# Performance work log

Hardware: AMD Instinct MI355X
Metric: run time of the kernel (lower is better)

Reference implementation:

```python
import jax, jax.numpy as jnp
import numpy as np

EPS_LN = 1e-5   # torch.nn.LayerNorm default eps
EPS_Q = 1e-5    # BitNetQuantizer eps
QMAX = 127.0    # 2**(8-1) - 1 for 8-bit activations


def _layernorm(v):
    # LayerNorm without affine params, biased variance (torch default)
    mu = jnp.mean(v, axis=-1, keepdims=True)
    var = jnp.var(v, axis=-1, keepdims=True)
    return (v - mu) / jnp.sqrt(var + EPS_LN)


def setup_inputs() -> dict:
    key = jax.random.key(0)
    k1, k2, k3 = jax.random.split(key, 3)
    B, S, DIN, DOUT = 4, 4096, 2048, 2048
    x = jax.random.normal(k1, (B, S, DIN), dtype=jnp.float32)
    # ternary weights in {-1, 0, +1}
    weight_ternary = jax.random.randint(k2, (DOUT, DIN), -1, 2, dtype=jnp.int32)
    # positive per-row scale (from_float uses a scalar expanded; per-row is the stored form)
    weight_scale = jax.random.uniform(k3, (DOUT,), dtype=jnp.float32, minval=0.01, maxval=0.05)
    return {"x": x, "weight_ternary": weight_ternary, "weight_scale": weight_scale}


def reference(x, weight_ternary, weight_scale):
    # input LayerNorm (no affine)
    xn = _layernorm(x)
    # 8-bit activation quantization: per-token absmax scale
    x_scale = jnp.clip(jnp.max(jnp.abs(xn), axis=-1, keepdims=True), EPS_Q, None) / QMAX
    x_quant = jnp.clip(jnp.round(xn / x_scale), -QMAX, QMAX)
    x_float = x_quant * x_scale  # [B, S, DIN]
    # dequantize ternary weights: [DOUT, DIN]
    w = weight_ternary.astype(jnp.float32) * weight_scale[:, None]
    # F.linear: x @ w.T
    out = jnp.einsum('bsi,oi->bso', x_float, w)
    # output LayerNorm (no affine)
    return _layernorm(out)
```

## Files before the change

### kernel.cpp

```cpp
#include <hip/hip_runtime.h>
#include <hip/hip_bf16.h>
#include <stdint.h>

using int32x4 = __attribute__((ext_vector_type(4))) int;

#define DIN 2048
#define DOUT 2048
#define NTOK 16384
#define KDIM 2048
#define NDIM 2048

#define BM 256
#define BN 256
#define BKB 64
#define NKT (KDIM / BKB)
#define TILEB (BM * BKB)

typedef const __attribute__((address_space(1))) void* gp_t;
typedef __attribute__((address_space(3))) void* lp_t;

__device__ __forceinline__ void gload16(const void* g, void* l) {
    __builtin_amdgcn_global_load_lds((gp_t)g, (lp_t)l, 16, 0, 0);
}

__global__ __launch_bounds__(256) void k_wconv(const int* __restrict__ wt,
                                               signed char* __restrict__ w8) {
    int i = blockIdx.x * 256 + threadIdx.x;
    int4 v = ((const int4*)wt)[i];
    char4 c;
    c.x = (signed char)v.x; c.y = (signed char)v.y;
    c.z = (signed char)v.z; c.w = (signed char)v.w;
    ((char4*)w8)[i] = c;
}

__global__ __launch_bounds__(256) void k_lnq(const float* __restrict__ x,
                                             signed char* __restrict__ xq,
                                             float* __restrict__ xscale) {
    __shared__ float sm[12];
    const int row = blockIdx.x;
    const int tid = threadIdx.x;
    const float* p = x + (size_t)row * DIN;
    const float4 v0 = ((const float4*)p)[tid * 2];
    const float4 v1 = ((const float4*)p)[tid * 2 + 1];
    float vv[8] = {v0.x, v0.y, v0.z, v0.w, v1.x, v1.y, v1.z, v1.w};
    float s = 0.f, ss = 0.f;
#pragma unroll
    for (int i = 0; i < 8; i++) { s += vv[i]; ss += vv[i] * vv[i]; }
#pragma unroll
    for (int o = 32; o; o >>= 1) { s += __shfl_down(s, o); ss += __shfl_down(ss, o); }
    const int wv = tid >> 6;
    if ((tid & 63) == 0) { sm[wv] = s; sm[4 + wv] = ss; }
    __syncthreads();
    s = sm[0] + sm[1] + sm[2] + sm[3];
    ss = sm[4] + sm[5] + sm[6] + sm[7];
    const float mu = s * (1.f / DIN);
    const float var = ss * (1.f / DIN) - mu * mu;
    const float rstd = 1.f / sqrtf(var + 1e-5f);
    float am = 0.f;
#pragma unroll
    for (int i = 0; i < 8; i++) am = fmaxf(am, fabsf(vv[i] - mu));
#pragma unroll
    for (int o = 32; o; o >>= 1) am = fmaxf(am, __shfl_down(am, o));
    __syncthreads();
    if ((tid & 63) == 0) sm[8 + wv] = am;
    __syncthreads();
    am = fmaxf(fmaxf(sm[8], sm[9]), fmaxf(sm[10], sm[11]));
    const float scale = fmaxf(am * rstd, 1e-5f) * (1.f / 127.f);
    union { signed char c[8]; int2 v; } u;
#pragma unroll
    for (int i = 0; i < 8; i++) {
        float xn = (vv[i] - mu) * rstd;
        float t = rintf(xn / scale);
        t = fminf(127.f, fmaxf(-127.f, t));
        u.c[i] = (signed char)t;
    }
    ((int2*)(xq + (size_t)row * DIN))[tid] = u.v;
    if (tid == 0) xscale[row] = scale;
}

#define MFMA4(I, AF) \
    acc[I][0] = __builtin_amdgcn_mfma_i32_16x16x64_i8(AF, b0, acc[I][0], 0, 0, 0); \
    acc[I][1] = __builtin_amdgcn_mfma_i32_16x16x64_i8(AF, b1, acc[I][1], 0, 0, 0); \
    acc[I][2] = __builtin_amdgcn_mfma_i32_16x16x64_i8(AF, b2, acc[I][2], 0, 0, 0); \
    acc[I][3] = __builtin_amdgcn_mfma_i32_16x16x64_i8(AF, b3, acc[I][3], 0, 0, 0);

#define SCHED __builtin_amdgcn_sched_barrier(0);
#define BAR   __builtin_amdgcn_s_barrier();

__global__ __launch_bounds__(512, 2) void k_gemm(const signed char* __restrict__ A,
                                                 const signed char* __restrict__ B,
                                                 const float* __restrict__ xs,
                                                 const float* __restrict__ wsc,
                                                 float* __restrict__ C) {
    __shared__ __align__(16) signed char lA[3][TILEB];
    __shared__ __align__(16) signed char lB[3][TILEB];
    __shared__ float s_xs[BM];
    __shared__ float s_ws[BN];

    const int tid = threadIdx.x;
    const int orig = blockIdx.x;
    const int bid = (orig & 7) * 64 + (orig >> 3);
    const int bm = bid >> 3;
    const int bn = bid & 7;

    const int lane = tid & 63;
    const int wave = tid >> 6;
    const int wm = wave >> 2;
    const int wn = wave & 3;
    const int lo = lane & 15;
    const int q  = lane >> 4;

    const int srow = tid >> 2;
    const int gch  = (tid & 3) ^ ((srow >> 1) & 3);
    const signed char* gA = A + (size_t)(bm * BM + srow) * KDIM + gch * 16;
    const signed char* gB = B + (size_t)(bn * BN + srow) * KDIM + gch * 16;
    const int dst = tid * 16;

    const int slot = (q ^ ((lo >> 1) & 3)) * 16;
    const int abase = (wm * 128 + lo) * BKB + slot;
    const int bbase = (wn * 64 + lo) * BKB + slot;

    if (tid < 256) s_xs[tid] = xs[bm * BM + tid];
    else           s_ws[tid - 256] = wsc[bn * BN + tid - 256];

#define STAGE_A(T, BUF) \
    gload16(gA + (T) * BKB,                        &lA[BUF][0] + dst); \
    gload16(gA + (T) * BKB + (size_t)128 * KDIM,   &lA[BUF][0] + dst + 8192);
#define STAGE_B(T, BUF) \
    gload16(gB + (T) * BKB,                        &lB[BUF][0] + dst); \
    gload16(gB + (T) * BKB + (size_t)128 * KDIM,   &lB[BUF][0] + dst + 8192);

    STAGE_A(0, 0) STAGE_B(0, 0)
    STAGE_A(1, 1) STAGE_B(1, 1)
    asm volatile("s_waitcnt vmcnt(0)" ::: "memory");
    SCHED BAR SCHED

    int32x4 acc[8][4];
#pragma unroll
    for (int i = 0; i < 8; i++)
#pragma unroll
        for (int j = 0; j < 4; j++) {
            int32x4 z = {0, 0, 0, 0};
            acc[i][j] = z;
        }

    int cur = 0, nx2 = 2;
    for (int t = 0; t < NKT; ++t) {
        const signed char* lAc = &lA[cur][0];
        const signed char* lBc = &lB[cur][0];
        int32x4 a0, a1, a2, a3, a4, a5, a6, a7, b0, b1, b2, b3;

        a0 = *(const int32x4*)(lAc + abase + 0 * 1024);
        a1 = *(const int32x4*)(lAc + abase + 1 * 1024);
        a2 = *(const int32x4*)(lAc + abase + 2 * 1024);
        a3 = *(const int32x4*)(lAc + abase + 3 * 1024);
        b0 = *(const int32x4*)(lBc + bbase + 0 * 1024);
        b1 = *(const int32x4*)(lBc + bbase + 1 * 1024);
        b2 = *(const int32x4*)(lBc + bbase + 2 * 1024);
        b3 = *(const int32x4*)(lBc + bbase + 3 * 1024);
        a4 = *(const int32x4*)(lAc + abase + 4 * 1024);
        a5 = *(const int32x4*)(lAc + abase + 5 * 1024);
        a6 = *(const int32x4*)(lAc + abase + 6 * 1024);
        a7 = *(const int32x4*)(lAc + abase + 7 * 1024);
        asm volatile("s_waitcnt vmcnt(0)" ::: "memory");
        SCHED
        BAR
        SCHED
        if (t + 2 < NKT) {
            STAGE_A(t + 2, nx2)
            STAGE_B(t + 2, nx2)
        }
        SCHED
        asm volatile("s_waitcnt lgkmcnt(4)" ::: "memory");
        SCHED
        __builtin_amdgcn_s_setprio(1);
        MFMA4(0, a0) MFMA4(1, a1) MFMA4(2, a2) MFMA4(3, a3)
        __builtin_amdgcn_s_setprio(0);
        SCHED
        asm volatile("s_waitcnt lgkmcnt(0)" ::: "memory");
        SCHED
        __builtin_amdgcn_s_setprio(1);
        MFMA4(4, a4) MFMA4(5, a5) MFMA4(6, a6) MFMA4(7, a7)
        __builtin_amdgcn_s_setprio(0);
        SCHED

        cur = (cur == 2) ? 0 : cur + 1;
        nx2 = (nx2 == 2) ? 0 : nx2 + 1;
    }

#pragma unroll
    for (int i = 0; i < 8; ++i) {
#pragma unroll
        for (int j = 0; j < 4; ++j) {
            const int ln = wn * 64 + j * 16 + lo;
            const float wsv = s_ws[ln];
            float* cp = C + (size_t)(bm * BM + wm * 128 + i * 16 + q * 4) * NDIM + bn * BN + ln;
#pragma unroll
            for (int r = 0; r < 4; ++r) {
                const int lm = wm * 128 + i * 16 + q * 4 + r;
                cp[(size_t)r * NDIM] = (float)acc[i][j][r] * s_xs[lm] * wsv;
            }
        }
    }
}

__global__ __launch_bounds__(256) void k_lnout(float* __restrict__ y) {
    __shared__ float sm[8];
    const int row = blockIdx.x;
    const int tid = threadIdx.x;
    float* p = y + (size_t)row * DOUT;
    float4 v0 = ((float4*)p)[tid * 2];
    float4 v1 = ((float4*)p)[tid * 2 + 1];
    float vv[8] = {v0.x, v0.y, v0.z, v0.w, v1.x, v1.y, v1.z, v1.w};
    float s = 0.f, ss = 0.f;
#pragma unroll
    for (int i = 0; i < 8; i++) { s += vv[i]; ss += vv[i] * vv[i]; }
#pragma unroll
    for (int o = 32; o; o >>= 1) { s += __shfl_down(s, o); ss += __shfl_down(ss, o); }
    const int wv = tid >> 6;
    if ((tid & 63) == 0) { sm[wv] = s; sm[4 + wv] = ss; }
    __syncthreads();
    s = sm[0] + sm[1] + sm[2] + sm[3];
    ss = sm[4] + sm[5] + sm[6] + sm[7];
    const float mu = s * (1.f / DOUT);
    const float var = ss * (1.f / DOUT) - mu * mu;
    const float rstd = 1.f / sqrtf(var + 1e-5f);
#pragma unroll
    for (int i = 0; i < 8; i++) vv[i] = (vv[i] - mu) * rstd;
    float4 o0, o1;
    o0.x = vv[0]; o0.y = vv[1]; o0.z = vv[2]; o0.w = vv[3];
    o1.x = vv[4]; o1.y = vv[5]; o1.z = vv[6]; o1.w = vv[7];
    ((float4*)p)[tid * 2] = o0;
    ((float4*)p)[tid * 2 + 1] = o1;
}

extern "C" void kernel_launch(void* const* d_in, const int* in_sizes, int n_in,
                              void* d_out, int out_size, void* d_ws, size_t ws_size,
                              hipStream_t stream) {
    const float* x = (const float*)d_in[0];
    const int* wt = (const int*)d_in[1];
    const float* wscale = (const float*)d_in[2];
    float* out = (float*)d_out;

    signed char* w8 = (signed char*)d_ws;
    signed char* xq = (signed char*)d_ws + (size_t)4 * 1024 * 1024;
    float* xs = (float*)((char*)d_ws + (size_t)36 * 1024 * 1024);

    k_wconv<<<(DOUT * DIN / 4) / 256, 256, 0, stream>>>(wt, w8);
    k_lnq<<<NTOK, 256, 0, stream>>>(x, xq, xs);
    k_gemm<<<(NTOK / BM) * (NDIM / BN), 512, 0, stream>>>(xq, w8, xs, wscale, out);
    k_lnout<<<NTOK, 256, 0, stream>>>(out);
}
```

Measured before the change: 157.9 us.

## Deepen GEMM LDS pipeline to four stages and prefetch next-tile fragments into registers

Raises the int8 GEMM's LDS ring from three to four buffers, so global loads are issued three tiles ahead and waited on with partial vmcnt instead of full drains. The loop is unrolled by two with ping-pong register sets. The first half of the A fragments and all B fragments for the next tile are read from LDS during the current tile, which overlaps LDS latency with MFMA work. In exchange it uses more LDS (128KB of tiles per block, which may limit the two-blocks-per-CU occupancy) and more VGPRs, and the manual waitcnt accounting is fragile.

```diff
diff --git a/kernel.cpp b/kernel.cpp
--- a/kernel.cpp
+++ b/kernel.cpp
@@ -78,22 +78,22 @@
     if (tid == 0) xscale[row] = scale;
 }
 
-#define MFMA4(I, AF) \
-    acc[I][0] = __builtin_amdgcn_mfma_i32_16x16x64_i8(AF, b0, acc[I][0], 0, 0, 0); \
-    acc[I][1] = __builtin_amdgcn_mfma_i32_16x16x64_i8(AF, b1, acc[I][1], 0, 0, 0); \
-    acc[I][2] = __builtin_amdgcn_mfma_i32_16x16x64_i8(AF, b2, acc[I][2], 0, 0, 0); \
-    acc[I][3] = __builtin_amdgcn_mfma_i32_16x16x64_i8(AF, b3, acc[I][3], 0, 0, 0);
-
 #define SCHED __builtin_amdgcn_sched_barrier(0);
 #define BAR   __builtin_amdgcn_s_barrier();
+
+#define MFMA4S(I, AF, S) \
+    acc[I][0] = __builtin_amdgcn_mfma_i32_16x16x64_i8(AF, pb##S##0, acc[I][0], 0, 0, 0); \
+    acc[I][1] = __builtin_amdgcn_mfma_i32_16x16x64_i8(AF, pb##S##1, acc[I][1], 0, 0, 0); \
+    acc[I][2] = __builtin_amdgcn_mfma_i32_16x16x64_i8(AF, pb##S##2, acc[I][2], 0, 0, 0); \
+    acc[I][3] = __builtin_amdgcn_mfma_i32_16x16x64_i8(AF, pb##S##3, acc[I][3], 0, 0, 0);
 
 __global__ __launch_bounds__(512, 2) void k_gemm(const signed char* __restrict__ A,
                                                  const signed char* __restrict__ B,
                                                  const float* __restrict__ xs,
                                                  const float* __restrict__ wsc,
                                                  float* __restrict__ C) {
-    __shared__ __align__(16) signed char lA[3][TILEB];
-    __shared__ __align__(16) signed char lB[3][TILEB];
+    __shared__ __align__(16) signed char lA[4][TILEB];
+    __shared__ __align__(16) signed char lB[4][TILEB];
     __shared__ float s_xs[BM];
     __shared__ float s_ws[BN];
 
@@ -124,16 +124,34 @@
     else           s_ws[tid - 256] = wsc[bn * BN + tid - 256];
 
 #define STAGE_A(T, BUF) \
-    gload16(gA + (T) * BKB,                        &lA[BUF][0] + dst); \
-    gload16(gA + (T) * BKB + (size_t)128 * KDIM,   &lA[BUF][0] + dst + 8192);
+    gload16(gA + (T) * BKB,                      &lA[BUF][0] + dst); \
+    gload16(gA + (T) * BKB + (size_t)128 * KDIM, &lA[BUF][0] + dst + 8192);
 #define STAGE_B(T, BUF) \
-    gload16(gB + (T) * BKB,                        &lB[BUF][0] + dst); \
-    gload16(gB + (T) * BKB + (size_t)128 * KDIM,   &lB[BUF][0] + dst + 8192);
+    gload16(gB + (T) * BKB,                      &lB[BUF][0] + dst); \
+    gload16(gB + (T) * BKB + (size_t)128 * KDIM, &lB[BUF][0] + dst + 8192);
 
     STAGE_A(0, 0) STAGE_B(0, 0)
     STAGE_A(1, 1) STAGE_B(1, 1)
-    asm volatile("s_waitcnt vmcnt(0)" ::: "memory");
+    STAGE_A(2, 2) STAGE_B(2, 2)
+    asm volatile("s_waitcnt vmcnt(8)" ::: "memory");
     SCHED BAR SCHED
+
+    int32x4 paA0, paA1, paA2, paA3, pbA0, pbA1, pbA2, pbA3;
+    int32x4 paB0, paB1, paB2, paB3, pbB0, pbB1, pbB2, pbB3;
+    int32x4 a4, a5, a6, a7;
+
+    {
+        const signed char* lAc = &lA[0][0];
+        const signed char* lBc = &lB[0][0];
+        pbA0 = *(const int32x4*)(lBc + bbase + 0 * 1024);
+        pbA1 = *(const int32x4*)(lBc + bbase + 1 * 1024);
+        pbA2 = *(const int32x4*)(lBc + bbase + 2 * 1024);
+        pbA3 = *(const int32x4*)(lBc + bbase + 3 * 1024);
+        paA0 = *(const int32x4*)(lAc + abase + 0 * 1024);
+        paA1 = *(const int32x4*)(lAc + abase + 1 * 1024);
+        paA2 = *(const int32x4*)(lAc + abase + 2 * 1024);
+        paA3 = *(const int32x4*)(lAc + abase + 3 * 1024);
+    }
 
     int32x4 acc[8][4];
 #pragma unroll
@@ -144,48 +162,47 @@
             acc[i][j] = z;
         }
 
-    int cur = 0, nx2 = 2;
-    for (int t = 0; t < NKT; ++t) {
-        const signed char* lAc = &lA[cur][0];
-        const signed char* lBc = &lB[cur][0];
-        int32x4 a0, a1, a2, a3, a4, a5, a6, a7, b0, b1, b2, b3;
-
-        a0 = *(const int32x4*)(lAc + abase + 0 * 1024);
-        a1 = *(const int32x4*)(lAc + abase + 1 * 1024);
-        a2 = *(const int32x4*)(lAc + abase + 2 * 1024);
-        a3 = *(const int32x4*)(lAc + abase + 3 * 1024);
-        b0 = *(const int32x4*)(lBc + bbase + 0 * 1024);
-        b1 = *(const int32x4*)(lBc + bbase + 1 * 1024);
-        b2 = *(const int32x4*)(lBc + bbase + 2 * 1024);
-        b3 = *(const int32x4*)(lBc + bbase + 3 * 1024);
-        a4 = *(const int32x4*)(lAc + abase + 4 * 1024);
-        a5 = *(const int32x4*)(lAc + abase + 5 * 1024);
-        a6 = *(const int32x4*)(lAc + abase + 6 * 1024);
-        a7 = *(const int32x4*)(lAc + abase + 7 * 1024);
-        asm volatile("s_waitcnt vmcnt(0)" ::: "memory");
-        SCHED
-        BAR
-        SCHED
-        if (t + 2 < NKT) {
-            STAGE_A(t + 2, nx2)
-            STAGE_B(t + 2, nx2)
-        }
-        SCHED
-        asm volatile("s_waitcnt lgkmcnt(4)" ::: "memory");
-        SCHED
-        __builtin_amdgcn_s_setprio(1);
-        MFMA4(0, a0) MFMA4(1, a1) MFMA4(2, a2) MFMA4(3, a3)
-        __builtin_amdgcn_s_setprio(0);
-        SCHED
-        asm volatile("s_waitcnt lgkmcnt(0)" ::: "memory");
-        SCHED
-        __builtin_amdgcn_s_setprio(1);
-        MFMA4(4, a4) MFMA4(5, a5) MFMA4(6, a6) MFMA4(7, a7)
-        __builtin_amdgcn_s_setprio(0);
-        SCHED
-
-        cur = (cur == 2) ? 0 : cur + 1;
-        nx2 = (nx2 == 2) ? 0 : nx2 + 1;
+#define ITER(T, CS, NS) do { \
+    const signed char* lAc = &lA[(T) & 3][0]; \
+    const signed char* lBn = &lB[((T) + 1) & 3][0]; \
+    const signed char* lAn = &lA[((T) + 1) & 3][0]; \
+    if ((T) + 2 < NKT) { asm volatile("s_waitcnt vmcnt(4)" ::: "memory"); } \
+    else               { asm volatile("s_waitcnt vmcnt(0)" ::: "memory"); } \
+    asm volatile("s_waitcnt lgkmcnt(0)" ::: "memory"); \
+    SCHED BAR SCHED \
+    if ((T) + 3 < NKT) { STAGE_A((T) + 3, ((T) + 3) & 3) STAGE_B((T) + 3, ((T) + 3) & 3) } \
+    a4 = *(const int32x4*)(lAc + abase + 4 * 1024); \
+    a5 = *(const int32x4*)(lAc + abase + 5 * 1024); \
+    a6 = *(const int32x4*)(lAc + abase + 6 * 1024); \
+    a7 = *(const int32x4*)(lAc + abase + 7 * 1024); \
+    if ((T) + 1 < NKT) { \
+        pb##NS##0 = *(const int32x4*)(lBn + bbase + 0 * 1024); \
+        pb##NS##1 = *(const int32x4*)(lBn + bbase + 1 * 1024); \
+        pb##NS##2 = *(const int32x4*)(lBn + bbase + 2 * 1024); \
+        pb##NS##3 = *(const int32x4*)(lBn + bbase + 3 * 1024); \
+        pa##NS##0 = *(const int32x4*)(lAn + abase + 0 * 1024); \
+        pa##NS##1 = *(const int32x4*)(lAn + abase + 1 * 1024); \
+        pa##NS##2 = *(const int32x4*)(lAn + abase + 2 * 1024); \
+        pa##NS##3 = *(const int32x4*)(lAn + abase + 3 * 1024); \
+    } \
+    SCHED \
+    __builtin_amdgcn_s_setprio(1); \
+    MFMA4S(0, pa##CS##0, CS) MFMA4S(1, pa##CS##1, CS) \
+    MFMA4S(2, pa##CS##2, CS) MFMA4S(3, pa##CS##3, CS) \
+    __builtin_amdgcn_s_setprio(0); \
+    SCHED \
+    if ((T) + 1 < NKT) { asm volatile("s_waitcnt lgkmcnt(8)" ::: "memory"); } \
+    else               { asm volatile("s_waitcnt lgkmcnt(0)" ::: "memory"); } \
+    SCHED \
+    __builtin_amdgcn_s_setprio(1); \
+    MFMA4S(4, a4, CS) MFMA4S(5, a5, CS) MFMA4S(6, a6, CS) MFMA4S(7, a7, CS) \
+    __builtin_amdgcn_s_setprio(0); \
+    SCHED \
+} while (0)
+
+    for (int t = 0; t < NKT; t += 2) {
+        ITER(t, A, B);
+        ITER(t + 1, B, A);
     }
 
 #pragma unroll
```

Result: slower. 174.1 us (+10.3%).
